# Performance work log

Hardware: AMD Instinct MI355X
Metric: run time of the kernel (lower is better)

The kernel has to match this reference:

```python
import jax, jax.numpy as jnp
import numpy as np

HIDDEN = 1024
HEADS = 16
HEAD_DIM = HIDDEN // HEADS


def setup_inputs() -> dict:
    key = jax.random.key(0)
    kx, kq, kk, kv, ko = jax.random.split(key, 5)
    s = 1.0 / np.sqrt(HIDDEN)
    return {
        "x": jax.random.normal(kx, (2, 2048, HIDDEN), dtype=jnp.float32),
        "Wq": jax.random.normal(kq, (HIDDEN, HIDDEN), dtype=jnp.float32) * s,
        "Wk": jax.random.normal(kk, (HIDDEN, HIDDEN), dtype=jnp.float32) * s,
        "Wv": jax.random.normal(kv, (HIDDEN, HIDDEN), dtype=jnp.float32) * s,
        "Wo": jax.random.normal(ko, (HIDDEN, HIDDEN), dtype=jnp.float32) * s,
    }


def reference(x, Wq, Wk, Wv, Wo):
    B, T, C = x.shape
    H, D = HEADS, HEAD_DIM
    # projections (torch Linear: y = x @ W.T); weights here stored as (out,in)==(C,C)
    q = (x @ Wq.T).reshape(B, T, H, D)
    k = (x @ Wk.T).reshape(B, T, H, D)
    v = (x @ Wv.T).reshape(B, T, H, D)
    scale = 1.0 / np.sqrt(D).astype(np.float32)
    # scores: (B,H,T,T)
    attn = jnp.einsum("bqhd,bkhd->bhqk", q, k) * scale
    causal = jnp.tril(jnp.ones((T, T), dtype=bool))  # keep lower triangle
    attn = jnp.where(causal, attn, -jnp.inf)
    attn = jax.nn.softmax(attn, axis=-1)
    out = jnp.einsum("bhqk,bkhd->bqhd", attn, v).reshape(B, T, C)
    return out @ Wo.T
```

## Files before the change

kernel.cpp:

```cpp
#include <hip/hip_runtime.h>
#include <cstdint>
#include <cstddef>

#define HID 1024
#define NH 16
#define HD 64
#define SEQ 2048
#define BATCH 2

typedef __attribute__((ext_vector_type(8))) short bf16x8;
typedef __attribute__((ext_vector_type(4))) short bf16x4;
typedef bf16x8 __attribute__((may_alias)) bf16x8_ma;
typedef bf16x4 __attribute__((may_alias)) bf16x4_ma;
typedef uint4 __attribute__((may_alias)) uint4_ma;
typedef __attribute__((ext_vector_type(4))) float f32x4;

__device__ __forceinline__ unsigned short f2bf(float f){
  unsigned u = __builtin_bit_cast(unsigned, f);
  u += 0x7fffu + ((u >> 16) & 1u);
  return (unsigned short)(u >> 16);
}

__device__ __forceinline__ unsigned cvtpk_bf16(float lo, float hi){
  unsigned r;
  asm("v_cvt_pk_bf16_f32 %0, %1, %2" : "=v"(r) : "v"(lo), "v"(hi));
  return r;
}

__device__ __forceinline__ void gll(const unsigned short* g, unsigned short* l){
  __builtin_amdgcn_global_load_lds(
      (const __attribute__((address_space(1))) unsigned int*)(g),
      (__attribute__((address_space(3))) unsigned int*)(l),
      16, 0, 0);
}

__global__ __launch_bounds__(256) void cvt_all(
    const float* __restrict__ x,  const float* __restrict__ wq,
    const float* __restrict__ wk, const float* __restrict__ wv,
    const float* __restrict__ wo,
    unsigned short* __restrict__ xb,  unsigned short* __restrict__ wqb,
    unsigned short* __restrict__ wkb, unsigned short* __restrict__ wvb,
    unsigned short* __restrict__ wob)
{
  const size_t NX = (size_t)BATCH*SEQ*HID;
  const size_t NW = (size_t)HID*HID;
  size_t i = ((size_t)blockIdx.x*256 + threadIdx.x)*4;
  const float* src; unsigned short* dst; size_t off;
  if (i < NX) { src = x; dst = xb; off = i; }
  else {
    size_t j = i - NX; int w = (int)(j >> 20); off = j & (NW-1);
    if      (w==0){ src=wq; dst=wqb; }
    else if (w==1){ src=wk; dst=wkb; }
    else if (w==2){ src=wv; dst=wvb; }
    else          { src=wo; dst=wob; }
  }
  float4 v = *(const float4*)(src+off);
  uint2 p;
  p.x = (unsigned)f2bf(v.x) | ((unsigned)f2bf(v.y)<<16);
  p.y = (unsigned)f2bf(v.z) | ((unsigned)f2bf(v.w)<<16);
  *(uint2*)(dst+off) = p;
}

__global__ __launch_bounds__(256) void gemm_qkv(
    const unsigned short* __restrict__ A,
    const unsigned short* __restrict__ Bq,
    const unsigned short* __restrict__ Bk,
    const unsigned short* __restrict__ Bv,
    unsigned short* __restrict__ Qh,
    unsigned short* __restrict__ Kh,
    unsigned short* __restrict__ Vh)
{
  __shared__ unsigned short S[16384];
  const int tid = threadIdx.x;
  const int w = tid >> 6, lane = tid & 63, l15 = lane & 15, quad = lane >> 4;
  const int wm = (w >> 1)*64, wn = (w & 1)*64;
  const int bm = blockIdx.y*128;
  const int which = blockIdx.x >> 3;
  const int bn = (blockIdx.x & 7)*128;
  const unsigned short* B = which==0 ? Bq : (which==1 ? Bk : Bv);
  unsigned short* C       = which==0 ? Qh : (which==1 ? Kh : Vh);
  const float cscale      = which==0 ? 0.18033688011112042f : 1.0f;
  const int lrow = lane >> 2, lcol = (lane & 3)*8;

  f32x4 acc[4][4] = {};

  {
    #pragma unroll
    for (int p=0;p<2;p++){
      int c = w*2 + p;
      gll(&A[(size_t)(bm + c*16 + lrow)*HID + lcol], &S[c*512]);
      gll(&B[(size_t)(bn + c*16 + lrow)*HID + lcol], &S[8192 + c*512]);
    }
  }
  __syncthreads();

  int cur = 0;
  for (int kb=0; kb<32; ++kb){
    if (kb < 31){
      unsigned short* Ad = S + (cur^1)*4096;
      unsigned short* Bd = S + 8192 + (cur^1)*4096;
      #pragma unroll
      for (int p=0;p<2;p++){
        int c = w*2 + p;
        gll(&A[(size_t)(bm + c*16 + lrow)*HID + (kb+1)*32 + lcol], &Ad[c*512]);
        gll(&B[(size_t)(bn + c*16 + lrow)*HID + (kb+1)*32 + lcol], &Bd[c*512]);
      }
    }
    const unsigned short* Ac = S + cur*4096;
    const unsigned short* Bc = S + 8192 + cur*4096;
    bf16x8 af[4], bfr[4];
    #pragma unroll
    for (int i=0;i<4;i++) af[i]  = *(const bf16x8*)(&Ac[(wm + i*16 + l15)*32 + quad*8]);
    #pragma unroll
    for (int j=0;j<4;j++) bfr[j] = *(const bf16x8*)(&Bc[(wn + j*16 + l15)*32 + quad*8]);
    #pragma unroll
    for (int i=0;i<4;i++)
      #pragma unroll
      for (int j=0;j<4;j++)
        acc[i][j] = __builtin_amdgcn_mfma_f32_16x16x32_bf16(af[i], bfr[j], acc[i][j], 0,0,0);
    __syncthreads();
    cur ^= 1;
  }

  #pragma unroll
  for (int i=0;i<4;i++)
    #pragma unroll
    for (int j=0;j<4;j++)
      #pragma unroll
      for (int r=0;r<4;r++){
        int row = wm + i*16 + quad*4 + r;
        int col = wn + j*16 + l15;
        unsigned off = (unsigned)(row*256 + col*2);
        *(unsigned short*)((char*)S + (off ^ ((unsigned)(row & 7) << 4))) =
            f2bf(acc[i][j][r]*cscale);
      }
  __syncthreads();
  #pragma unroll
  for (int pass=0; pass<8; ++pass){
    int tr    = pass*16 + (tid >> 4);
    int half  = (tid >> 3) & 1;
    int blkin = tid & 7;
    unsigned off = (unsigned)(tr*256 + half*128 + blkin*16);
    uint4 v = *(const uint4_ma*)((const char*)S + (off ^ ((unsigned)(tr & 7) << 4)));
    int m = bm + tr, b = m >> 11, t = m & (SEQ-1);
    int h = (bn >> 6) + half;
    *(uint4*)(&C[(((size_t)(b*NH + h))*SEQ + t)*HD + blkin*8]) = v;
  }
}

__global__ __launch_bounds__(256) void gemm_out(
    const unsigned short* __restrict__ A,
    const unsigned short* __restrict__ B,
    float* __restrict__ C)
{
  __shared__ unsigned short As[8192];
  __shared__ unsigned short Bs[4096];
  const int tid = threadIdx.x;
  const int w = tid >> 6, lane = tid & 63, l15 = lane & 15, quad = lane >> 4;
  const int wm = (w >> 1)*64, wn = (w & 1)*32;
  const int bm = blockIdx.y*128, bn = blockIdx.x*64;
  const int lrow = lane >> 2, lcol = (lane & 3)*8;

  f32x4 acc[4][2] = {};
  for (int kb=0; kb<16; ++kb){
    __syncthreads();
    #pragma unroll
    for (int p=0;p<4;p++){
      int c = p*4 + w;
      int h = c >> 3, rb = c & 7;
      gll(&A[(size_t)(bm + rb*16 + lrow)*HID + kb*64 + h*32 + lcol], &As[h*4096 + rb*512]);
    }
    #pragma unroll
    for (int p=0;p<2;p++){
      int c = p*4 + w;
      int h = c >> 2, rb = c & 3;
      gll(&B[(size_t)(bn + rb*16 + lrow)*HID + kb*64 + h*32 + lcol], &Bs[h*2048 + rb*512]);
    }
    __syncthreads();
    #pragma unroll
    for (int kc=0;kc<2;kc++){
      bf16x8 af[4], bfr[2];
      #pragma unroll
      for (int i=0;i<4;i++) af[i]  = *(const bf16x8*)(&As[kc*4096 + (wm + i*16 + l15)*32 + quad*8]);
      #pragma unroll
      for (int j=0;j<2;j++) bfr[j] = *(const bf16x8*)(&Bs[kc*2048 + (wn + j*16 + l15)*32 + quad*8]);
      #pragma unroll
      for (int i=0;i<4;i++)
        #pragma unroll
        for (int j=0;j<2;j++)
          acc[i][j] = __builtin_amdgcn_mfma_f32_16x16x32_bf16(af[i], bfr[j], acc[i][j], 0,0,0);
    }
  }
  #pragma unroll
  for (int i=0;i<4;i++)
    #pragma unroll
    for (int j=0;j<2;j++)
      #pragma unroll
      for (int r=0;r<4;r++){
        int m = bm + wm + i*16 + quad*4 + r;
        int n = bn + wn + j*16 + l15;
        C[(size_t)m*HID + n] = acc[i][j][r];
      }
}

__global__ __launch_bounds__(256) void vtrans(
    const unsigned short* __restrict__ Vh, unsigned short* __restrict__ VhT)
{
  __shared__ unsigned short t[64*66];
  const int bh = blockIdx.y, tb = blockIdx.x;
  const int tid = threadIdx.x;
  const unsigned short* src = Vh + ((size_t)bh*SEQ + tb*64)*HD;
  #pragma unroll
  for (int i=0;i<2;i++){
    int c = i*256 + tid; int r = c >> 3, c8 = (c & 7)*8;
    unsigned short tmp[8];
    *(uint4*)tmp = *(const uint4*)(&src[r*HD + c8]);
    #pragma unroll
    for (int j=0;j<8;j++) t[(c8+j)*66 + r] = tmp[j];
  }
  __syncthreads();
  unsigned short* dst = VhT + (size_t)bh*HD*SEQ + tb*64;
  #pragma unroll
  for (int i=0;i<2;i++){
    int c = i*256 + tid; int d = c >> 3, t8 = (c & 7)*8;
    uint4 v; unsigned short* pv = (unsigned short*)&v;
    #pragma unroll
    for (int j=0;j<8;j++) pv[j] = t[d*66 + t8 + j];
    *(uint4*)(&dst[(size_t)d*SEQ + t8]) = v;
  }
}

__global__ __launch_bounds__(256, 4) void attn(
    const unsigned short* __restrict__ Qh,
    const unsigned short* __restrict__ Kh,
    const unsigned short* __restrict__ VhT,
    unsigned short* __restrict__ Ao)
{
  __shared__ unsigned short QP[4096];
  __shared__ unsigned short Ks[2][4096];
  __shared__ unsigned short Vt[2][4096];

  const int bh = blockIdx.x;
  const int y  = blockIdx.y;
  const int a = y & 7, bb = y >> 3;
  const int qb = (bb & 1) ? (7 - a)*4 + bb : a*4 + bb;
  const int tid = threadIdx.x;
  const int w = tid >> 6, lane = tid & 63, l15 = lane & 15, quad = lane >> 4;
  const int lrow = lane >> 2, lcol = (lane & 3)*8;

  const size_t base = (size_t)bh * SEQ * HD;
  const unsigned short* Qg  = Qh + base + (size_t)qb*64*HD;
  const unsigned short* VTg = VhT + base;
  unsigned short* Psw = QP + w*1024;
  const unsigned swz = (unsigned)(l15 & 7) << 4;

  #pragma unroll
  for (int p=0;p<2;p++){
    int c = w*2 + p;
    gll(&Qg[(size_t)((c&3)*16 + lrow)*HD + (c>>2)*32 + lcol], &QP[(c>>2)*2048 + (c&3)*512]);
  }
  {
    const unsigned short* Kg = Kh + base;
    if (w < 2){
      #pragma unroll
      for (int p=0;p<4;p++){ int cc = w*4 + p;
        gll(&Kg[(size_t)((cc&3)*16 + lrow)*HD + (cc>>2)*32 + lcol], &Ks[0][(cc>>2)*2048 + (cc&3)*512]); }
    } else {
      #pragma unroll
      for (int p=0;p<4;p++){ int cc = (w-2)*4 + p;
        gll(&VTg[(size_t)((cc&3)*16 + lrow)*SEQ + (cc>>2)*32 + lcol], &Vt[0][(cc>>2)*2048 + (cc&3)*512]); }
    }
  }
  __syncthreads();
  bf16x8 qfrag[2];
  #pragma unroll
  for (int kc=0;kc<2;kc++)
    qfrag[kc] = *(const bf16x8*)(&QP[kc*2048 + (w*16 + l15)*32 + quad*8]);
  __syncthreads();

  f32x4 lacc = {0.f, 0.f, 0.f, 0.f};
  f32x4 oacc[4] = {};
  const int qrow = qb*64 + w*16 + l15;
  int cur = 0;

  for (int kb=0; kb<=qb; ++kb){
    if (kb < qb){
      const unsigned short* Kg2 = Kh + base + (size_t)(kb+1)*64*HD;
      unsigned short* Kd = Ks[cur^1];
      unsigned short* Vd = Vt[cur^1];
      if (w < 2){
        #pragma unroll
        for (int p=0;p<4;p++){ int cc = w*4 + p;
          gll(&Kg2[(size_t)((cc&3)*16 + lrow)*HD + (cc>>2)*32 + lcol], &Kd[(cc>>2)*2048 + (cc&3)*512]); }
      } else {
        #pragma unroll
        for (int p=0;p<4;p++){ int cc = (w-2)*4 + p;
          gll(&VTg[(size_t)((cc&3)*16 + lrow)*SEQ + (size_t)(kb+1)*64 + (cc>>2)*32 + lcol], &Vd[(cc>>2)*2048 + (cc&3)*512]); }
      }
    }

    const unsigned short* Ksc = Ks[cur];
    f32x4 s[4] = {};
    #pragma unroll
    for (int cb=0;cb<4;cb++)
      #pragma unroll
      for (int kc=0;kc<2;kc++){
        bf16x8 kfr = *(const bf16x8*)(&Ksc[kc*2048 + (cb*16 + l15)*32 + quad*8]);
        s[cb] = __builtin_amdgcn_mfma_f32_16x16x32_bf16(kfr, qfrag[kc], s[cb], 0,0,0);
      }

    if (kb == qb){
      #pragma unroll
      for (int cb=0;cb<4;cb++)
        #pragma unroll
        for (int r=0;r<4;r++){
          int t = kb*64 + cb*16 + quad*4 + r;
          if (t > qrow) s[cb][r] = -1e30f;
        }
    }
    #pragma unroll
    for (int cb=0;cb<4;cb++)
      #pragma unroll
      for (int r=0;r<4;r++)
        s[cb][r] = exp2f(s[cb][r]);
    lacc += (s[0] + s[1]) + (s[2] + s[3]);

    #pragma unroll
    for (int cb=0;cb<4;cb++){
      uint2 d2;
      d2.x = cvtpk_bf16(s[cb][0], s[cb][1]);
      d2.y = cvtpk_bf16(s[cb][2], s[cb][3]);
      *(bf16x4_ma*)((char*)Psw + (((unsigned)(l15*128 + cb*32 + quad*8)) ^ swz)) =
          __builtin_bit_cast(bf16x4, d2);
    }
    asm volatile("" ::: "memory");
    bf16x8 pa[2];
    #pragma unroll
    for (int kc=0;kc<2;kc++)
      pa[kc] = *(const bf16x8_ma*)((const char*)Psw + (((unsigned)(l15*128 + kc*64 + quad*16)) ^ swz));

    const unsigned short* Vtc = Vt[cur];
    #pragma unroll
    for (int db=0;db<4;db++)
      #pragma unroll
      for (int kc=0;kc<2;kc++){
        bf16x8 vfr = *(const bf16x8*)(&Vtc[kc*2048 + (db*16 + l15)*32 + quad*8]);
        oacc[db] = __builtin_amdgcn_mfma_f32_16x16x32_bf16(pa[kc], vfr, oacc[db], 0,0,0);
      }

    if (kb < qb) __syncthreads();
    cur ^= 1;
  }

  float l = (lacc[0] + lacc[1]) + (lacc[2] + lacc[3]);
  l += __shfl_xor(l, 16);
  l += __shfl_xor(l, 32);
  float inv[4];
  #pragma unroll
  for (int r=0;r<4;r++)
    inv[r] = 1.0f / __shfl(l, quad*4 + r);

  const int b = bh >> 4, h = bh & (NH-1);
  #pragma unroll
  for (int db=0;db<4;db++)
    #pragma unroll
    for (int r=0;r<4;r++){
      int t = qb*64 + w*16 + quad*4 + r;
      int col = h*HD + db*16 + l15;
      Ao[((size_t)b*SEQ + t)*HID + col] = f2bf(oacc[db][r] * inv[r]);
    }
}

extern "C" void kernel_launch(void* const* d_in, const int* in_sizes, int n_in,
                              void* d_out, int out_size, void* d_ws, size_t ws_size,
                              hipStream_t stream)
{
  const float* x  = (const float*)d_in[0];
  const float* Wq = (const float*)d_in[1];
  const float* Wk = (const float*)d_in[2];
  const float* Wv = (const float*)d_in[3];
  const float* Wo = (const float*)d_in[4];

  unsigned short* xb  = (unsigned short*)d_ws;
  unsigned short* wqb = xb  + (size_t)4*1024*1024;
  unsigned short* wkb = wqb + (size_t)1024*1024;
  unsigned short* wvb = wkb + (size_t)1024*1024;
  unsigned short* wob = wvb + (size_t)1024*1024;
  unsigned short* Qh  = wob + (size_t)1024*1024;
  unsigned short* Kh  = Qh  + (size_t)4*1024*1024;
  unsigned short* Vh  = Kh  + (size_t)4*1024*1024;
  unsigned short* VhT = Vh  + (size_t)4*1024*1024;
  unsigned short* Ao  = xb;

  cvt_all<<<8192, 256, 0, stream>>>(x, Wq, Wk, Wv, Wo, xb, wqb, wkb, wvb, wob);

  gemm_qkv<<<dim3(24, 32), 256, 0, stream>>>(xb, wqb, wkb, wvb, Qh, Kh, Vh);

  vtrans<<<dim3(SEQ/64, BATCH*NH), 256, 0, stream>>>(Vh, VhT);

  attn<<<dim3(BATCH*NH, SEQ/64), 256, 0, stream>>>(Qh, Kh, VhT, Ao);

  gemm_out<<<dim3(16, 32), 256, 0, stream>>>(Ao, wob, (float*)d_out);
}
```

Before: 181.3 us.

## Fuse V transpose into QKV GEMM epilogue and pair causal query blocks per CTA

The QKV GEMM epilogue now writes V straight into the transposed (head, dim, seq) layout by reading its swizzled shared-memory tile column-wise, so the separate vtrans kernel and its round trip through global memory go away. The attention kernel now handles two query blocks per CTA (y and 31-y) sequentially, which balances causal work across CTAs and halves the grid. In exchange, the V epilogue does scalar LDS reads that may hit bank conflicts, and the smaller attention grid leaves fewer CTAs to hide latency.

```diff
diff --git a/kernel.cpp b/kernel.cpp
--- a/kernel.cpp
+++ b/kernel.cpp
@@ -68,7 +68,7 @@
     const unsigned short* __restrict__ Bv,
     unsigned short* __restrict__ Qh,
     unsigned short* __restrict__ Kh,
-    unsigned short* __restrict__ Vh)
+    unsigned short* __restrict__ VhT)
 {
   __shared__ unsigned short S[16384];
   const int tid = threadIdx.x;
@@ -78,7 +78,7 @@
   const int which = blockIdx.x >> 3;
   const int bn = (blockIdx.x & 7)*128;
   const unsigned short* B = which==0 ? Bq : (which==1 ? Bk : Bv);
-  unsigned short* C       = which==0 ? Qh : (which==1 ? Kh : Vh);
+  unsigned short* C       = which==0 ? Qh : (which==1 ? Kh : VhT);
   const float cscale      = which==0 ? 0.18033688011112042f : 1.0f;
   const int lrow = lane >> 2, lcol = (lane & 3)*8;
 
@@ -135,16 +135,36 @@
             f2bf(acc[i][j][r]*cscale);
       }
   __syncthreads();
-  #pragma unroll
-  for (int pass=0; pass<8; ++pass){
-    int tr    = pass*16 + (tid >> 4);
-    int half  = (tid >> 3) & 1;
-    int blkin = tid & 7;
-    unsigned off = (unsigned)(tr*256 + half*128 + blkin*16);
-    uint4 v = *(const uint4_ma*)((const char*)S + (off ^ ((unsigned)(tr & 7) << 4)));
-    int m = bm + tr, b = m >> 11, t = m & (SEQ-1);
-    int h = (bn >> 6) + half;
-    *(uint4*)(&C[(((size_t)(b*NH + h))*SEQ + t)*HD + blkin*8]) = v;
+  if (which < 2){
+    #pragma unroll
+    for (int pass=0; pass<8; ++pass){
+      int tr    = pass*16 + (tid >> 4);
+      int hf    = (tid >> 3) & 1;
+      int blkin = tid & 7;
+      unsigned off = (unsigned)(tr*256 + hf*128 + blkin*16);
+      uint4 v = *(const uint4_ma*)((const char*)S + (off ^ ((unsigned)(tr & 7) << 4)));
+      int m = bm + tr, b = m >> 11, t = m & (SEQ-1);
+      int h = (bn >> 6) + hf;
+      *(uint4*)(&C[(((size_t)(b*NH + h))*SEQ + t)*HD + blkin*8]) = v;
+    }
+  } else {
+    const int b = bm >> 11, tb = bm & (SEQ-1);
+    #pragma unroll
+    for (int pass=0; pass<8; ++pass){
+      int idx  = pass*256 + tid;
+      int dcol = idx & 127;
+      int tc   = idx >> 7;
+      unsigned short tmp[8];
+      #pragma unroll
+      for (int j=0;j<8;j++){
+        int r = tc*8 + j;
+        unsigned off = (unsigned)(r*256 + dcol*2) ^ ((unsigned)j << 4);
+        tmp[j] = *(const unsigned short*)((const char*)S + off);
+      }
+      int hh = (bn >> 6) + (dcol >> 6);
+      int d  = dcol & 63;
+      *(uint4*)(&C[(((size_t)(b*NH + hh))*HD + d)*SEQ + tb + tc*8]) = *(uint4_ma*)tmp;
+    }
   }
 }
 
@@ -203,33 +223,6 @@
       }
 }
 
-__global__ __launch_bounds__(256) void vtrans(
-    const unsigned short* __restrict__ Vh, unsigned short* __restrict__ VhT)
-{
-  __shared__ unsigned short t[64*66];
-  const int bh = blockIdx.y, tb = blockIdx.x;
-  const int tid = threadIdx.x;
-  const unsigned short* src = Vh + ((size_t)bh*SEQ + tb*64)*HD;
-  #pragma unroll
-  for (int i=0;i<2;i++){
-    int c = i*256 + tid; int r = c >> 3, c8 = (c & 7)*8;
-    unsigned short tmp[8];
-    *(uint4*)tmp = *(const uint4*)(&src[r*HD + c8]);
-    #pragma unroll
-    for (int j=0;j<8;j++) t[(c8+j)*66 + r] = tmp[j];
-  }
-  __syncthreads();
-  unsigned short* dst = VhT + (size_t)bh*HD*SEQ + tb*64;
-  #pragma unroll
-  for (int i=0;i<2;i++){
-    int c = i*256 + tid; int d = c >> 3, t8 = (c & 7)*8;
-    uint4 v; unsigned short* pv = (unsigned short*)&v;
-    #pragma unroll
-    for (int j=0;j<8;j++) pv[j] = t[d*66 + t8 + j];
-    *(uint4*)(&dst[(size_t)d*SEQ + t8]) = v;
-  }
-}
-
 __global__ __launch_bounds__(256, 4) void attn(
     const unsigned short* __restrict__ Qh,
     const unsigned short* __restrict__ Kh,
@@ -242,133 +235,138 @@
 
   const int bh = blockIdx.x;
   const int y  = blockIdx.y;
-  const int a = y & 7, bb = y >> 3;
-  const int qb = (bb & 1) ? (7 - a)*4 + bb : a*4 + bb;
   const int tid = threadIdx.x;
   const int w = tid >> 6, lane = tid & 63, l15 = lane & 15, quad = lane >> 4;
   const int lrow = lane >> 2, lcol = (lane & 3)*8;
 
   const size_t base = (size_t)bh * SEQ * HD;
-  const unsigned short* Qg  = Qh + base + (size_t)qb*64*HD;
   const unsigned short* VTg = VhT + base;
   unsigned short* Psw = QP + w*1024;
   const unsigned swz = (unsigned)(l15 & 7) << 4;
-
-  #pragma unroll
-  for (int p=0;p<2;p++){
-    int c = w*2 + p;
-    gll(&Qg[(size_t)((c&3)*16 + lrow)*HD + (c>>2)*32 + lcol], &QP[(c>>2)*2048 + (c&3)*512]);
-  }
-  {
-    const unsigned short* Kg = Kh + base;
-    if (w < 2){
-      #pragma unroll
-      for (int p=0;p<4;p++){ int cc = w*4 + p;
-        gll(&Kg[(size_t)((cc&3)*16 + lrow)*HD + (cc>>2)*32 + lcol], &Ks[0][(cc>>2)*2048 + (cc&3)*512]); }
-    } else {
-      #pragma unroll
-      for (int p=0;p<4;p++){ int cc = (w-2)*4 + p;
-        gll(&VTg[(size_t)((cc&3)*16 + lrow)*SEQ + (cc>>2)*32 + lcol], &Vt[0][(cc>>2)*2048 + (cc&3)*512]); }
-    }
-  }
-  __syncthreads();
-  bf16x8 qfrag[2];
-  #pragma unroll
-  for (int kc=0;kc<2;kc++)
-    qfrag[kc] = *(const bf16x8*)(&QP[kc*2048 + (w*16 + l15)*32 + quad*8]);
-  __syncthreads();
-
-  f32x4 lacc = {0.f, 0.f, 0.f, 0.f};
-  f32x4 oacc[4] = {};
-  const int qrow = qb*64 + w*16 + l15;
-  int cur = 0;
-
-  for (int kb=0; kb<=qb; ++kb){
-    if (kb < qb){
-      const unsigned short* Kg2 = Kh + base + (size_t)(kb+1)*64*HD;
-      unsigned short* Kd = Ks[cur^1];
-      unsigned short* Vd = Vt[cur^1];
+  const int b = bh >> 4, h = bh & (NH-1);
+
+  #pragma unroll 1
+  for (int hf=0; hf<2; ++hf){
+    const int qb = hf ? (31 - y) : y;
+    const unsigned short* Qg = Qh + base + (size_t)qb*64*HD;
+
+    __syncthreads();
+
+    #pragma unroll
+    for (int p=0;p<2;p++){
+      int c = w*2 + p;
+      gll(&Qg[(size_t)((c&3)*16 + lrow)*HD + (c>>2)*32 + lcol], &QP[(c>>2)*2048 + (c&3)*512]);
+    }
+    {
+      const unsigned short* Kg = Kh + base;
       if (w < 2){
         #pragma unroll
         for (int p=0;p<4;p++){ int cc = w*4 + p;
-          gll(&Kg2[(size_t)((cc&3)*16 + lrow)*HD + (cc>>2)*32 + lcol], &Kd[(cc>>2)*2048 + (cc&3)*512]); }
+          gll(&Kg[(size_t)((cc&3)*16 + lrow)*HD + (cc>>2)*32 + lcol], &Ks[0][(cc>>2)*2048 + (cc&3)*512]); }
       } else {
         #pragma unroll
         for (int p=0;p<4;p++){ int cc = (w-2)*4 + p;
-          gll(&VTg[(size_t)((cc&3)*16 + lrow)*SEQ + (size_t)(kb+1)*64 + (cc>>2)*32 + lcol], &Vd[(cc>>2)*2048 + (cc&3)*512]); }
-      }
-    }
-
-    const unsigned short* Ksc = Ks[cur];
-    f32x4 s[4] = {};
-    #pragma unroll
-    for (int cb=0;cb<4;cb++)
-      #pragma unroll
-      for (int kc=0;kc<2;kc++){
-        bf16x8 kfr = *(const bf16x8*)(&Ksc[kc*2048 + (cb*16 + l15)*32 + quad*8]);
-        s[cb] = __builtin_amdgcn_mfma_f32_16x16x32_bf16(kfr, qfrag[kc], s[cb], 0,0,0);
-      }
-
-    if (kb == qb){
+          gll(&VTg[(size_t)((cc&3)*16 + lrow)*SEQ + (cc>>2)*32 + lcol], &Vt[0][(cc>>2)*2048 + (cc&3)*512]); }
+      }
+    }
+    __syncthreads();
+    bf16x8 qfrag[2];
+    #pragma unroll
+    for (int kc=0;kc<2;kc++)
+      qfrag[kc] = *(const bf16x8*)(&QP[kc*2048 + (w*16 + l15)*32 + quad*8]);
+    __syncthreads();
+
+    f32x4 lacc = {0.f, 0.f, 0.f, 0.f};
+    f32x4 oacc[4] = {};
+    const int qrow = qb*64 + w*16 + l15;
+    int cur = 0;
+
+    for (int kb=0; kb<=qb; ++kb){
+      if (kb < qb){
+        const unsigned short* Kg2 = Kh + base + (size_t)(kb+1)*64*HD;
+        unsigned short* Kd = Ks[cur^1];
+        unsigned short* Vd = Vt[cur^1];
+        if (w < 2){
+          #pragma unroll
+          for (int p=0;p<4;p++){ int cc = w*4 + p;
+            gll(&Kg2[(size_t)((cc&3)*16 + lrow)*HD + (cc>>2)*32 + lcol], &Kd[(cc>>2)*2048 + (cc&3)*512]); }
+        } else {
+          #pragma unroll
+          for (int p=0;p<4;p++){ int cc = (w-2)*4 + p;
+            gll(&VTg[(size_t)((cc&3)*16 + lrow)*SEQ + (size_t)(kb+1)*64 + (cc>>2)*32 + lcol], &Vd[(cc>>2)*2048 + (cc&3)*512]); }
+        }
+      }
+
+      const unsigned short* Ksc = Ks[cur];
+      f32x4 s[4] = {};
       #pragma unroll
       for (int cb=0;cb<4;cb++)
         #pragma unroll
-        for (int r=0;r<4;r++){
-          int t = kb*64 + cb*16 + quad*4 + r;
-          if (t > qrow) s[cb][r] = -1e30f;
+        for (int kc=0;kc<2;kc++){
+          bf16x8 kfr = *(const bf16x8*)(&Ksc[kc*2048 + (cb*16 + l15)*32 + quad*8]);
+          s[cb] = __builtin_amdgcn_mfma_f32_16x16x32_bf16(kfr, qfrag[kc], s[cb], 0,0,0);
         }
-    }
-    #pragma unroll
-    for (int cb=0;cb<4;cb++)
-      #pragma unroll
-      for (int r=0;r<4;r++)
-        s[cb][r] = exp2f(s[cb][r]);
-    lacc += (s[0] + s[1]) + (s[2] + s[3]);
-
-    #pragma unroll
-    for (int cb=0;cb<4;cb++){
-      uint2 d2;
-      d2.x = cvtpk_bf16(s[cb][0], s[cb][1]);
-      d2.y = cvtpk_bf16(s[cb][2], s[cb][3]);
-      *(bf16x4_ma*)((char*)Psw + (((unsigned)(l15*128 + cb*32 + quad*8)) ^ swz)) =
-          __builtin_bit_cast(bf16x4, d2);
-    }
-    asm volatile("" ::: "memory");
-    bf16x8 pa[2];
-    #pragma unroll
-    for (int kc=0;kc<2;kc++)
-      pa[kc] = *(const bf16x8_ma*)((const char*)Psw + (((unsigned)(l15*128 + kc*64 + quad*16)) ^ swz));
-
-    const unsigned short* Vtc = Vt[cur];
+
+      if (kb == qb){
+        #pragma unroll
+        for (int cb=0;cb<4;cb++)
+          #pragma unroll
+          for (int r=0;r<4;r++){
+            int t = kb*64 + cb*16 + quad*4 + r;
+            if (t > qrow) s[cb][r] = -1e30f;
+          }
+      }
+      #pragma unroll
+      for (int cb=0;cb<4;cb++)
+        #pragma unroll
+        for (int r=0;r<4;r++)
+          s[cb][r] = exp2f(s[cb][r]);
+      lacc += (s[0] + s[1]) + (s[2] + s[3]);
+
+      #pragma unroll
+      for (int cb=0;cb<4;cb++){
+        uint2 d2;
+        d2.x = cvtpk_bf16(s[cb][0], s[cb][1]);
+        d2.y = cvtpk_bf16(s[cb][2], s[cb][3]);
+        *(bf16x4_ma*)((char*)Psw + (((unsigned)(l15*128 + cb*32 + quad*8)) ^ swz)) =
+            __builtin_bit_cast(bf16x4, d2);
+      }
+      asm volatile("" ::: "memory");
+      bf16x8 pa[2];
+      #pragma unroll
+      for (int kc=0;kc<2;kc++)
+        pa[kc] = *(const bf16x8_ma*)((const char*)Psw + (((unsigned)(l15*128 + kc*64 + quad*16)) ^ swz));
+
+      const unsigned short* Vtc = Vt[cur];
+      #pragma unroll
+      for (int db=0;db<4;db++)
+        #pragma unroll
+        for (int kc=0;kc<2;kc++){
+          bf16x8 vfr = *(const bf16x8*)(&Vtc[kc*2048 + (db*16 + l15)*32 + quad*8]);
+          oacc[db] = __builtin_amdgcn_mfma_f32_16x16x32_bf16(pa[kc], vfr, oacc[db], 0,0,0);
+        }
+
+      if (kb < qb) __syncthreads();
+      cur ^= 1;
+    }
+
+    float l = (lacc[0] + lacc[1]) + (lacc[2] + lacc[3]);
+    l += __shfl_xor(l, 16);
+    l += __shfl_xor(l, 32);
+    float inv[4];
+    #pragma unroll
+    for (int r=0;r<4;r++)
+      inv[r] = 1.0f / __shfl(l, quad*4 + r);
+
     #pragma unroll
     for (int db=0;db<4;db++)
       #pragma unroll
-      for (int kc=0;kc<2;kc++){
-        bf16x8 vfr = *(const bf16x8*)(&Vtc[kc*2048 + (db*16 + l15)*32 + quad*8]);
-        oacc[db] = __builtin_amdgcn_mfma_f32_16x16x32_bf16(pa[kc], vfr, oacc[db], 0,0,0);
-      }
-
-    if (kb < qb) __syncthreads();
-    cur ^= 1;
-  }
-
-  float l = (lacc[0] + lacc[1]) + (lacc[2] + lacc[3]);
-  l += __shfl_xor(l, 16);
-  l += __shfl_xor(l, 32);
-  float inv[4];
-  #pragma unroll
-  for (int r=0;r<4;r++)
-    inv[r] = 1.0f / __shfl(l, quad*4 + r);
-
-  const int b = bh >> 4, h = bh & (NH-1);
-  #pragma unroll
-  for (int db=0;db<4;db++)
-    #pragma unroll
-    for (int r=0;r<4;r++){
-      int t = qb*64 + w*16 + quad*4 + r;
-      int col = h*HD + db*16 + l15;
-      Ao[((size_t)b*SEQ + t)*HID + col] = f2bf(oacc[db][r] * inv[r]);
-    }
+      for (int r=0;r<4;r++){
+        int t = qb*64 + w*16 + quad*4 + r;
+        int col = h*HD + db*16 + l15;
+        Ao[((size_t)b*SEQ + t)*HID + col] = f2bf(oacc[db][r] * inv[r]);
+      }
+  }
 }
 
 extern "C" void kernel_launch(void* const* d_in, const int* in_sizes, int n_in,
@@ -394,11 +392,9 @@
 
   cvt_all<<<8192, 256, 0, stream>>>(x, Wq, Wk, Wv, Wo, xb, wqb, wkb, wvb, wob);
 
-  gemm_qkv<<<dim3(24, 32), 256, 0, stream>>>(xb, wqb, wkb, wvb, Qh, Kh, Vh);
-
-  vtrans<<<dim3(SEQ/64, BATCH*NH), 256, 0, stream>>>(Vh, VhT);
-
-  attn<<<dim3(BATCH*NH, SEQ/64), 256, 0, stream>>>(Qh, Kh, VhT, Ao);
+  gemm_qkv<<<dim3(24, 32), 256, 0, stream>>>(xb, wqb, wkb, wvb, Qh, Kh, VhT);
+
+  attn<<<dim3(BATCH*NH, 16), 256, 0, stream>>>(Qh, Kh, VhT, Ao);
 
   gemm_out<<<dim3(16, 32), 256, 0, stream>>>(Ao, wob, (float*)d_out);
 }
```

Measured after the change: 178.7 us. About the same (-1.4%).
